# Kernel tuning notes

Measured on AMD Instinct MI355X. Metric: run time of the kernel, lower is better.

## Reference

```python
import jax, jax.numpy as jnp
import numpy as np

NUM_USERS = 200_000
NUM_ITEMS = 100_000
N = NUM_USERS + NUM_ITEMS
D = 32
E = 9_600_000
N_LAYERS = 3


def setup_inputs() -> dict:
    key = jax.random.key(0)
    k1, k2, k3, k4, k5 = jax.random.split(key, 5)
    rows = jax.random.randint(k1, (E,), 0, N, dtype=jnp.int32)
    cols = jax.random.randint(k2, (E,), 0, N, dtype=jnp.int32)
    # normalized-adjacency-like positive values
    vals = jax.random.uniform(k3, (E,), dtype=jnp.float32) * 0.05
    # xavier-uniform-ish embedding init
    bound = float(np.sqrt(6.0 / (NUM_USERS + D)))
    user_w = jax.random.uniform(k4, (NUM_USERS, D), dtype=jnp.float32,
                                minval=-bound, maxval=bound)
    bound_i = float(np.sqrt(6.0 / (NUM_ITEMS + D)))
    item_w = jax.random.uniform(k5, (NUM_ITEMS, D), dtype=jnp.float32,
                                minval=-bound_i, maxval=bound_i)
    return {"rows": rows, "cols": cols, "vals": vals,
            "user_w": user_w, "item_w": item_w}


def _spmm(rows, cols, vals, x):
    # A_hat @ x for COO A_hat: gather source features, scale, scatter-add to rows.
    msgs = vals[:, None] * x[cols]                 # [E, D]
    return jax.ops.segment_sum(msgs, rows, num_segments=N)  # [N, D]


def reference(rows, cols, vals, user_w, item_w):
    x0 = jnp.concatenate([user_w, item_w], axis=0)  # [N, D]
    x = x0
    acc = x0
    for _ in range(N_LAYERS):
        x = _spmm(rows, cols, vals, x)
        acc = acc + x
    x_mean = acc / (N_LAYERS + 1)                   # mean over layer stack
    users = x_mean[:NUM_USERS]
    items = x_mean[NUM_USERS:]
    return (users, items)
```

## Files before the change

### kernel.cpp

```cpp
#include <hip/hip_runtime.h>
#include <hip/hip_fp16.h>
#include <stdint.h>

#define NUM_USERS 200000
#define NUM_ITEMS 100000
#define NN (NUM_USERS + NUM_ITEMS)
#define D 32
#define NE 9600000
#define TOTAL (NN * D)

#define RPB2 128
#define B2 ((NN + RPB2 - 1) / RPB2)
#define CAP 5120

#define CSH 12
#define NC ((NN + (1 << CSH) - 1) >> CSH)
#define FPC 32
#define BPC 9

#define TPB_A 1024
#define EPT 16
#define EPB_A (TPB_A * EPT)

#define TPB_H 1024
#define EPT_H 32
#define EPB_H (TPB_H * EPT_H)
#define NB_H ((NE + EPB_H - 1) / EPB_H)

__global__ __launch_bounds__(256) void init_x_acc(
    const float4* __restrict__ user_w, const float4* __restrict__ item_w,
    ushort4* __restrict__ xh, float4* __restrict__ acc) {
    int i = blockIdx.x * 256 + threadIdx.x;
    const int total4 = TOTAL / 4;
    const int ub4 = (NUM_USERS * D) / 4;
    if (i < total4) {
        float4 v = (i < ub4) ? user_w[i] : item_w[i - ub4];
        acc[i] = v;
        ushort4 h;
        h.x = __half_as_ushort(__float2half(v.x));
        h.y = __half_as_ushort(__float2half(v.y));
        h.z = __half_as_ushort(__float2half(v.z));
        h.w = __half_as_ushort(__float2half(v.w));
        xh[i] = h;
    }
}

__global__ __launch_bounds__(TPB_H) void bucket_hist(
    const int4* __restrict__ rows4, int* __restrict__ bcounts) {
    __shared__ int hist[B2];
    int tid = threadIdx.x;
    for (int i = tid; i < B2; i += TPB_H) hist[i] = 0;
    __syncthreads();
    int base4 = blockIdx.x * (EPB_H / 4);
    #pragma unroll
    for (int k = 0; k < EPT_H / 4; ++k) {
        int i4 = base4 + k * TPB_H + tid;
        if (i4 < NE / 4) {
            int4 r = rows4[i4];
            atomicAdd(&hist[r.x >> 7], 1);
            atomicAdd(&hist[r.y >> 7], 1);
            atomicAdd(&hist[r.z >> 7], 1);
            atomicAdd(&hist[r.w >> 7], 1);
        }
    }
    __syncthreads();
    for (int b = tid; b < B2; b += TPB_H) {
        int c = hist[b];
        if (c) atomicAdd(&bcounts[b], c);
    }
}

__global__ __launch_bounds__(1024) void scan_buckets(
    const int* __restrict__ bcounts, int* __restrict__ bstart,
    int* __restrict__ bfill, int* __restrict__ cfill) {
    __shared__ int lds[1024];
    int t = threadIdx.x;
    int v[4];
    int s = 0;
    #pragma unroll
    for (int k = 0; k < 4; ++k) {
        int b = t * 4 + k;
        v[k] = (b < B2) ? bcounts[b] : 0;
        s += v[k];
    }
    lds[t] = s;
    __syncthreads();
    for (int off = 1; off < 1024; off <<= 1) {
        int u = (t >= off) ? lds[t - off] : 0;
        __syncthreads();
        lds[t] += u;
        __syncthreads();
    }
    int ex = lds[t] - s;
    #pragma unroll
    for (int k = 0; k < 4; ++k) {
        int b = t * 4 + k;
        if (b < B2) {
            bstart[b] = ex;
            bfill[b] = ex;
            if ((b & (FPC - 1)) == 0) cfill[b >> 5] = ex;
        }
        ex += v[k];
    }
    if (t == 1023) bstart[B2] = ex;
}

__global__ __launch_bounds__(TPB_A) void partition_coarse(
    const int4* __restrict__ rows4, const int4* __restrict__ cols4,
    const float4* __restrict__ vals4, int* __restrict__ cfill,
    int2* __restrict__ temp1) {
    __shared__ int2 stage[EPB_A];
    __shared__ int hist[NC];
    __shared__ int bnd[NC + 1];
    __shared__ int dlt[NC];
    __shared__ int sc[128];
    int tid = threadIdx.x;
    if (tid < NC) hist[tid] = 0;
    __syncthreads();

    int base4 = blockIdx.x * (EPB_A / 4);
    int keys[EPT]; int vls[EPT]; int crk[EPT];

    #pragma unroll
    for (int k = 0; k < EPT / 4; ++k) {
        int i4 = base4 + k * TPB_A + tid;
        if (i4 < NE / 4) {
            int4 r = rows4[i4];
            int4 c = cols4[i4];
            float4 v = vals4[i4];
            int c0 = r.x >> CSH, c1 = r.y >> CSH, c2 = r.z >> CSH, c3 = r.w >> CSH;
            keys[k*4+0] = ((r.x & 4095) << 19) | c.x; vls[k*4+0] = __float_as_int(v.x);
            crk[k*4+0] = (c0 << 13) | atomicAdd(&hist[c0], 1);
            keys[k*4+1] = ((r.y & 4095) << 19) | c.y; vls[k*4+1] = __float_as_int(v.y);
            crk[k*4+1] = (c1 << 13) | atomicAdd(&hist[c1], 1);
            keys[k*4+2] = ((r.z & 4095) << 19) | c.z; vls[k*4+2] = __float_as_int(v.z);
            crk[k*4+2] = (c2 << 13) | atomicAdd(&hist[c2], 1);
            keys[k*4+3] = ((r.w & 4095) << 19) | c.w; vls[k*4+3] = __float_as_int(v.w);
            crk[k*4+3] = (c3 << 13) | atomicAdd(&hist[c3], 1);
        }
    }
    __syncthreads();
    if (tid < 128) sc[tid] = (tid < NC) ? hist[tid] : 0;
    __syncthreads();
    #pragma unroll
    for (int off = 1; off < 128; off <<= 1) {
        int u = (tid >= off && tid < 128) ? sc[tid - off] : 0;
        __syncthreads();
        if (tid < 128) sc[tid] += u;
        __syncthreads();
    }
    if (tid < NC) {
        int cnt = hist[tid];
        int ex = sc[tid] - cnt;
        bnd[tid] = ex;
        dlt[tid] = (cnt ? atomicAdd(&cfill[tid], cnt) : 0) - ex;
    }
    if (tid == 0) bnd[NC] = sc[NC - 1];
    __syncthreads();
    #pragma unroll
    for (int k = 0; k < EPT / 4; ++k) {
        int i4 = base4 + k * TPB_A + tid;
        if (i4 < NE / 4) {
            #pragma unroll
            for (int j = 0; j < 4; ++j) {
                int e = k * 4 + j;
                int p = bnd[crk[e] >> 13] + (crk[e] & 0x1FFF);
                stage[p] = make_int2(keys[e], vls[e]);
            }
        }
    }
    __syncthreads();
    int ntot = bnd[NC];
    for (int j = tid; j < ntot; j += TPB_A) {
        int lo = 0, hi = NC;
        while (hi - lo > 1) { int mid = (lo + hi) >> 1; if (bnd[mid] <= j) lo = mid; else hi = mid; }
        temp1[j + dlt[lo]] = stage[j];
    }
}

__global__ __launch_bounds__(TPB_A) void partition_fine(
    const int2* __restrict__ temp1, const int* __restrict__ bstart,
    int* __restrict__ bfill, int2* __restrict__ colval) {
    __shared__ int2 stage[EPB_A];
    __shared__ int hist[FPC];
    __shared__ int bnd[FPC + 1];
    __shared__ int dlt[FPC];
    __shared__ int sc[FPC];
    int c = blockIdx.x / BPC;
    int seg = blockIdx.x % BPC;
    int cs = bstart[c * FPC];
    int ce = bstart[min((c + 1) * FPC, B2)];
    int base = cs + seg * EPB_A;
    int n = ce - base;
    if (n <= 0) return;
    if (n > EPB_A) n = EPB_A;
    int tid = threadIdx.x;
    if (tid < FPC) hist[tid] = 0;
    __syncthreads();
    int keys[EPT]; int vls[EPT]; int frk[EPT];
    #pragma unroll
    for (int k = 0; k < EPT; ++k) {
        int idx = k * TPB_A + tid;
        if (idx < n) {
            int2 e = temp1[base + idx];
            int f = (e.x >> 26) & 31;
            keys[k] = e.x; vls[k] = e.y;
            frk[k] = (f << 13) | atomicAdd(&hist[f], 1);
        }
    }
    __syncthreads();
    if (tid < FPC) sc[tid] = hist[tid];
    __syncthreads();
    #pragma unroll
    for (int off = 1; off < FPC; off <<= 1) {
        int u = (tid >= off && tid < FPC) ? sc[tid - off] : 0;
        __syncthreads();
        if (tid < FPC) sc[tid] += u;
        __syncthreads();
    }
    if (tid < FPC) {
        int cnt = hist[tid];
        int ex = sc[tid] - cnt;
        bnd[tid] = ex;
        dlt[tid] = (cnt ? atomicAdd(&bfill[c * FPC + tid], cnt) : 0) - ex;
    }
    if (tid == 0) bnd[FPC] = sc[FPC - 1];
    __syncthreads();
    #pragma unroll
    for (int k = 0; k < EPT; ++k) {
        int idx = k * TPB_A + tid;
        if (idx < n) {
            int p = bnd[frk[k] >> 13] + (frk[k] & 0x1FFF);
            int rl = (keys[k] >> 19) & 127;
            stage[p] = make_int2((rl << 19) | (keys[k] & 0x7FFFF), vls[k]);
        }
    }
    __syncthreads();
    for (int j = tid; j < n; j += TPB_A) {
        int lo = 0, hi = FPC;
        while (hi - lo > 1) { int mid = (lo + hi) >> 1; if (bnd[mid] <= j) lo = mid; else hi = mid; }
        colval[j + dlt[lo]] = stage[j];
    }
}

__global__ __launch_bounds__(256) void sort_bucket2(
    const int* __restrict__ bstart, int* __restrict__ row_start,
    int2* __restrict__ colval, int2* __restrict__ scratch) {
    __shared__ int2 stage[CAP];
    __shared__ int lstart[RPB2];
    __shared__ int lfill[RPB2];
    int b = blockIdx.x;
    int row0 = b * RPB2;
    int rcount = NN - row0; if (rcount > RPB2) rcount = RPB2;
    int tid = threadIdx.x;
    int s = bstart[b];
    int count = bstart[b + 1] - s;

    if (tid < RPB2) lfill[tid] = 0;
    __syncthreads();

    for (int i = tid; i < count; i += 256) {
        int rl = colval[s + i].x >> 19;
        atomicAdd(&lfill[rl], 1);
    }
    __syncthreads();

    int val = (tid < RPB2) ? lfill[tid] : 0;
    if (tid < RPB2) lstart[tid] = val;
    __syncthreads();
    for (int off = 1; off < RPB2; off <<= 1) {
        int u = (tid >= off && tid < RPB2) ? lstart[tid - off] : 0;
        __syncthreads();
        if (tid < RPB2) lstart[tid] += u;
        __syncthreads();
    }
    int ex = (tid < RPB2) ? lstart[tid] - val : 0;
    if (tid < RPB2) {
        lstart[tid] = ex;
        lfill[tid] = 0;
        if (tid < rcount) row_start[row0 + tid] = s + ex;
    }
    if (b == 0 && tid == 0) row_start[NN] = NE;
    __syncthreads();

    if (count <= CAP) {
        for (int i = tid; i < count; i += 256) {
            int2 e = colval[s + i];
            int rl = e.x >> 19;
            int pos = lstart[rl] + atomicAdd(&lfill[rl], 1);
            stage[pos] = make_int2(e.x & 0x7FFFF, e.y);
        }
        __syncthreads();
        for (int i = tid; i < count; i += 256) colval[s + i] = stage[i];
    } else {
        for (int i = tid; i < count; i += 256) scratch[s + i] = colval[s + i];
        __syncthreads();
        for (int i = tid; i < count; i += 256) {
            int2 e = scratch[s + i];
            int rl = e.x >> 19;
            int pos = lstart[rl] + atomicAdd(&lfill[rl], 1);
            colval[s + pos] = make_int2(e.x & 0x7FFFF, e.y);
        }
    }
}

template <bool LAST>
__global__ __launch_bounds__(256) void spmm_csr(
    const int* __restrict__ row_start, const int2* __restrict__ colval,
    const __half* __restrict__ xh, __half* __restrict__ yh,
    float* __restrict__ acc) {
    int lane = threadIdx.x & 63;
    int grp = lane >> 3;
    int fq = lane & 7;
    int row = (blockIdx.x * 256 + threadIdx.x) >> 6;
    if (row >= NN) return;
    int s = row_start[row];
    int e = row_start[row + 1];
    if (s == e) {
        if (lane < 8) {
            size_t idx = (size_t)row * D + lane * 4;
            if (!LAST) *(uint2*)(yh + idx) = make_uint2(0u, 0u);
            float4 av = *(const float4*)(acc + idx);
            if (LAST) { av.x *= 0.25f; av.y *= 0.25f; av.z *= 0.25f; av.w *= 0.25f; }
            *(float4*)(acc + idx) = av;
        }
        return;
    }
    float a0 = 0.f, a1 = 0.f, a2 = 0.f, a3 = 0.f;
    float b0 = 0.f, b1 = 0.f, b2 = 0.f, b3 = 0.f;
    int i = s;
    for (; i + 16 <= e; i += 16) {
        int2 cvA = colval[i + grp];
        int2 cvB = colval[i + 8 + grp];
        uint2 hA = *(const uint2*)(xh + (size_t)cvA.x * D + fq * 4);
        uint2 hB = *(const uint2*)(xh + (size_t)cvB.x * D + fq * 4);
        float vA = __int_as_float(cvA.y);
        float vB = __int_as_float(cvB.y);
        float2 fA0 = __half22float2(*(__half2*)&hA.x);
        float2 fA1 = __half22float2(*(__half2*)&hA.y);
        float2 fB0 = __half22float2(*(__half2*)&hB.x);
        float2 fB1 = __half22float2(*(__half2*)&hB.y);
        a0 += vA * fA0.x; a1 += vA * fA0.y; a2 += vA * fA1.x; a3 += vA * fA1.y;
        b0 += vB * fB0.x; b1 += vB * fB0.y; b2 += vB * fB1.x; b3 += vB * fB1.y;
    }
    if (i < e) {
        int iA = i + grp;
        int iB = i + 8 + grp;
        int cA = (iA < e) ? iA : (e - 1);
        int cB = (iB < e) ? iB : (e - 1);
        int2 cvA = colval[cA];
        int2 cvB = colval[cB];
        uint2 hA = *(const uint2*)(xh + (size_t)cvA.x * D + fq * 4);
        uint2 hB = *(const uint2*)(xh + (size_t)cvB.x * D + fq * 4);
        float vA = (iA < e) ? __int_as_float(cvA.y) : 0.f;
        float vB = (iB < e) ? __int_as_float(cvB.y) : 0.f;
        float2 fA0 = __half22float2(*(__half2*)&hA.x);
        float2 fA1 = __half22float2(*(__half2*)&hA.y);
        float2 fB0 = __half22float2(*(__half2*)&hB.x);
        float2 fB1 = __half22float2(*(__half2*)&hB.y);
        a0 += vA * fA0.x; a1 += vA * fA0.y; a2 += vA * fA1.x; a3 += vA * fA1.y;
        b0 += vB * fB0.x; b1 += vB * fB0.y; b2 += vB * fB1.x; b3 += vB * fB1.y;
    }
    a0 += b0; a1 += b1; a2 += b2; a3 += b3;
    #pragma unroll
    for (int m = 8; m <= 32; m <<= 1) {
        a0 += __shfl_xor(a0, m, 64);
        a1 += __shfl_xor(a1, m, 64);
        a2 += __shfl_xor(a2, m, 64);
        a3 += __shfl_xor(a3, m, 64);
    }
    if (lane < 8) {
        size_t idx = (size_t)row * D + lane * 4;
        if (!LAST) {
            __half2 h01 = __float22half2_rn(make_float2(a0, a1));
            __half2 h23 = __float22half2_rn(make_float2(a2, a3));
            *(uint2*)(yh + idx) =
                make_uint2(*(uint32_t*)&h01, *(uint32_t*)&h23);
        }
        float4 av = *(const float4*)(acc + idx);
        av.x += a0; av.y += a1; av.z += a2; av.w += a3;
        if (LAST) { av.x *= 0.25f; av.y *= 0.25f; av.z *= 0.25f; av.w *= 0.25f; }
        *(float4*)(acc + idx) = av;
    }
}

extern "C" void kernel_launch(void* const* d_in, const int* in_sizes, int n_in,
                              void* d_out, int out_size, void* d_ws, size_t ws_size,
                              hipStream_t stream) {
    const int*   rows   = (const int*)d_in[0];
    const int*   cols   = (const int*)d_in[1];
    const float* vals   = (const float*)d_in[2];
    const float* user_w = (const float*)d_in[3];
    const float* item_w = (const float*)d_in[4];

    float* acc = (float*)d_out;

    __half* xh = (__half*)d_ws;
    __half* yh = xh + (size_t)TOTAL;
    int2*  temp1 = (int2*)d_ws;
    int2*  colval = (int2*)((char*)d_ws + 2ull * (size_t)TOTAL * sizeof(float));
    int*   bcounts = (int*)(colval + (size_t)NE);
    int*   bstart = bcounts + B2;
    int*   bfill = bstart + (B2 + 1);
    int*   cfill = bfill + B2;
    int*   row_start = cfill + NC;

    const int vec_blocks   = (TOTAL / 4 + 255) / 256;
    const int partA_blocks = (NE + EPB_A - 1) / EPB_A;
    const int partF_blocks = NC * BPC;
    const int row_blocks   = (NN + 3) / 4;

    hipMemsetAsync(bcounts, 0, (size_t)B2 * sizeof(int), stream);
    bucket_hist<<<NB_H, TPB_H, 0, stream>>>((const int4*)rows, bcounts);
    scan_buckets<<<1, 1024, 0, stream>>>(bcounts, bstart, bfill, cfill);
    partition_coarse<<<partA_blocks, TPB_A, 0, stream>>>(
        (const int4*)rows, (const int4*)cols, (const float4*)vals, cfill, temp1);
    partition_fine<<<partF_blocks, TPB_A, 0, stream>>>(
        (const int2*)temp1, bstart, bfill, colval);
    sort_bucket2<<<B2, 256, 0, stream>>>(bstart, row_start, colval, temp1);

    init_x_acc<<<vec_blocks, 256, 0, stream>>>(
        (const float4*)user_w, (const float4*)item_w, (ushort4*)xh, (float4*)acc);

    spmm_csr<false><<<row_blocks, 256, 0, stream>>>(row_start, colval, xh, yh, acc);
    spmm_csr<false><<<row_blocks, 256, 0, stream>>>(row_start, colval, yh, xh, acc);
    spmm_csr<true ><<<row_blocks, 256, 0, stream>>>(row_start, colval, xh, yh, acc);
}
```

Baseline: 826.2 us.

## Store per-layer fp16 outputs and compute layer mean in a final kernel

SpMM layers no longer read-modify-write an fp32 accumulator. Each layer writes its own fp16 output buffer, and a new finalize kernel sums the four layers and scales by 1/4. The gather loop is widened to process 32 edges per iteration with nontemporal loads for column/value pairs. This cuts per-layer accumulator traffic and raises memory-level parallelism. In exchange, the initial embeddings are now rounded to fp16 before the mean, and an extra kernel launch is added.

```diff
diff --git a/kernel.cpp b/kernel.cpp
--- a/kernel.cpp
+++ b/kernel.cpp
@@ -27,21 +27,20 @@
 #define EPB_H (TPB_H * EPT_H)
 #define NB_H ((NE + EPB_H - 1) / EPB_H)
 
-__global__ __launch_bounds__(256) void init_x_acc(
+__global__ __launch_bounds__(256) void init_x0(
     const float4* __restrict__ user_w, const float4* __restrict__ item_w,
-    ushort4* __restrict__ xh, float4* __restrict__ acc) {
+    ushort4* __restrict__ x0h) {
     int i = blockIdx.x * 256 + threadIdx.x;
     const int total4 = TOTAL / 4;
     const int ub4 = (NUM_USERS * D) / 4;
     if (i < total4) {
         float4 v = (i < ub4) ? user_w[i] : item_w[i - ub4];
-        acc[i] = v;
         ushort4 h;
         h.x = __half_as_ushort(__float2half(v.x));
         h.y = __half_as_ushort(__float2half(v.y));
         h.z = __half_as_ushort(__float2half(v.z));
         h.w = __half_as_ushort(__float2half(v.w));
-        xh[i] = h;
+        x0h[i] = h;
     }
 }
 
@@ -304,11 +303,13 @@
     }
 }
 
-template <bool LAST>
+__device__ __forceinline__ float2 h2f(uint32_t u) {
+    return __half22float2(*(__half2*)&u);
+}
+
 __global__ __launch_bounds__(256) void spmm_csr(
     const int* __restrict__ row_start, const int2* __restrict__ colval,
-    const __half* __restrict__ xh, __half* __restrict__ yh,
-    float* __restrict__ acc) {
+    const __half* __restrict__ xh, __half* __restrict__ yh) {
     int lane = threadIdx.x & 63;
     int grp = lane >> 3;
     int fq = lane & 7;
@@ -316,52 +317,60 @@
     if (row >= NN) return;
     int s = row_start[row];
     int e = row_start[row + 1];
-    if (s == e) {
-        if (lane < 8) {
-            size_t idx = (size_t)row * D + lane * 4;
-            if (!LAST) *(uint2*)(yh + idx) = make_uint2(0u, 0u);
-            float4 av = *(const float4*)(acc + idx);
-            if (LAST) { av.x *= 0.25f; av.y *= 0.25f; av.z *= 0.25f; av.w *= 0.25f; }
-            *(float4*)(acc + idx) = av;
-        }
-        return;
-    }
+    const int64_t* cv8 = (const int64_t*)colval;
     float a0 = 0.f, a1 = 0.f, a2 = 0.f, a3 = 0.f;
-    float b0 = 0.f, b1 = 0.f, b2 = 0.f, b3 = 0.f;
     int i = s;
-    for (; i + 16 <= e; i += 16) {
-        int2 cvA = colval[i + grp];
-        int2 cvB = colval[i + 8 + grp];
-        uint2 hA = *(const uint2*)(xh + (size_t)cvA.x * D + fq * 4);
-        uint2 hB = *(const uint2*)(xh + (size_t)cvB.x * D + fq * 4);
-        float vA = __int_as_float(cvA.y);
-        float vB = __int_as_float(cvB.y);
-        float2 fA0 = __half22float2(*(__half2*)&hA.x);
-        float2 fA1 = __half22float2(*(__half2*)&hA.y);
-        float2 fB0 = __half22float2(*(__half2*)&hB.x);
-        float2 fB1 = __half22float2(*(__half2*)&hB.y);
-        a0 += vA * fA0.x; a1 += vA * fA0.y; a2 += vA * fA1.x; a3 += vA * fA1.y;
-        b0 += vB * fB0.x; b1 += vB * fB0.y; b2 += vB * fB1.x; b3 += vB * fB1.y;
+    for (; i + 32 <= e; i += 32) {
+        int64_t p0 = __builtin_nontemporal_load(&cv8[i + grp]);
+        int64_t p1 = __builtin_nontemporal_load(&cv8[i + 8 + grp]);
+        int64_t p2 = __builtin_nontemporal_load(&cv8[i + 16 + grp]);
+        int64_t p3 = __builtin_nontemporal_load(&cv8[i + 24 + grp]);
+        uint2 h0 = *(const uint2*)(xh + (size_t)(uint32_t)p0 * D + fq * 4);
+        uint2 h1 = *(const uint2*)(xh + (size_t)(uint32_t)p1 * D + fq * 4);
+        uint2 h2 = *(const uint2*)(xh + (size_t)(uint32_t)p2 * D + fq * 4);
+        uint2 h3 = *(const uint2*)(xh + (size_t)(uint32_t)p3 * D + fq * 4);
+        float v0 = __int_as_float((int)(p0 >> 32));
+        float v1 = __int_as_float((int)(p1 >> 32));
+        float v2 = __int_as_float((int)(p2 >> 32));
+        float v3 = __int_as_float((int)(p3 >> 32));
+        float2 f;
+        f = h2f(h0.x); a0 += v0 * f.x; a1 += v0 * f.y;
+        f = h2f(h0.y); a2 += v0 * f.x; a3 += v0 * f.y;
+        f = h2f(h1.x); a0 += v1 * f.x; a1 += v1 * f.y;
+        f = h2f(h1.y); a2 += v1 * f.x; a3 += v1 * f.y;
+        f = h2f(h2.x); a0 += v2 * f.x; a1 += v2 * f.y;
+        f = h2f(h2.y); a2 += v2 * f.x; a3 += v2 * f.y;
+        f = h2f(h3.x); a0 += v3 * f.x; a1 += v3 * f.y;
+        f = h2f(h3.y); a2 += v3 * f.x; a3 += v3 * f.y;
     }
     if (i < e) {
-        int iA = i + grp;
-        int iB = i + 8 + grp;
-        int cA = (iA < e) ? iA : (e - 1);
-        int cB = (iB < e) ? iB : (e - 1);
-        int2 cvA = colval[cA];
-        int2 cvB = colval[cB];
-        uint2 hA = *(const uint2*)(xh + (size_t)cvA.x * D + fq * 4);
-        uint2 hB = *(const uint2*)(xh + (size_t)cvB.x * D + fq * 4);
-        float vA = (iA < e) ? __int_as_float(cvA.y) : 0.f;
-        float vB = (iB < e) ? __int_as_float(cvB.y) : 0.f;
-        float2 fA0 = __half22float2(*(__half2*)&hA.x);
-        float2 fA1 = __half22float2(*(__half2*)&hA.y);
-        float2 fB0 = __half22float2(*(__half2*)&hB.x);
-        float2 fB1 = __half22float2(*(__half2*)&hB.y);
-        a0 += vA * fA0.x; a1 += vA * fA0.y; a2 += vA * fA1.x; a3 += vA * fA1.y;
-        b0 += vB * fB0.x; b1 += vB * fB0.y; b2 += vB * fB1.x; b3 += vB * fB1.y;
-    }
-    a0 += b0; a1 += b1; a2 += b2; a3 += b3;
+        int last = e - 1;
+        int i0 = i + grp,      c0 = (i0 < e) ? i0 : last;
+        int i1 = i + 8 + grp,  c1 = (i1 < e) ? i1 : last;
+        int i2 = i + 16 + grp, c2 = (i2 < e) ? i2 : last;
+        int i3 = i + 24 + grp, c3 = (i3 < e) ? i3 : last;
+        int64_t p0 = __builtin_nontemporal_load(&cv8[c0]);
+        int64_t p1 = __builtin_nontemporal_load(&cv8[c1]);
+        int64_t p2 = __builtin_nontemporal_load(&cv8[c2]);
+        int64_t p3 = __builtin_nontemporal_load(&cv8[c3]);
+        uint2 h0 = *(const uint2*)(xh + (size_t)(uint32_t)p0 * D + fq * 4);
+        uint2 h1 = *(const uint2*)(xh + (size_t)(uint32_t)p1 * D + fq * 4);
+        uint2 h2 = *(const uint2*)(xh + (size_t)(uint32_t)p2 * D + fq * 4);
+        uint2 h3 = *(const uint2*)(xh + (size_t)(uint32_t)p3 * D + fq * 4);
+        float v0 = (i0 < e) ? __int_as_float((int)(p0 >> 32)) : 0.f;
+        float v1 = (i1 < e) ? __int_as_float((int)(p1 >> 32)) : 0.f;
+        float v2 = (i2 < e) ? __int_as_float((int)(p2 >> 32)) : 0.f;
+        float v3 = (i3 < e) ? __int_as_float((int)(p3 >> 32)) : 0.f;
+        float2 f;
+        f = h2f(h0.x); a0 += v0 * f.x; a1 += v0 * f.y;
+        f = h2f(h0.y); a2 += v0 * f.x; a3 += v0 * f.y;
+        f = h2f(h1.x); a0 += v1 * f.x; a1 += v1 * f.y;
+        f = h2f(h1.y); a2 += v1 * f.x; a3 += v1 * f.y;
+        f = h2f(h2.x); a0 += v2 * f.x; a1 += v2 * f.y;
+        f = h2f(h2.y); a2 += v2 * f.x; a3 += v2 * f.y;
+        f = h2f(h3.x); a0 += v3 * f.x; a1 += v3 * f.y;
+        f = h2f(h3.y); a2 += v3 * f.x; a3 += v3 * f.y;
+    }
     #pragma unroll
     for (int m = 8; m <= 32; m <<= 1) {
         a0 += __shfl_xor(a0, m, 64);
@@ -371,17 +380,30 @@
     }
     if (lane < 8) {
         size_t idx = (size_t)row * D + lane * 4;
-        if (!LAST) {
-            __half2 h01 = __float22half2_rn(make_float2(a0, a1));
-            __half2 h23 = __float22half2_rn(make_float2(a2, a3));
-            *(uint2*)(yh + idx) =
-                make_uint2(*(uint32_t*)&h01, *(uint32_t*)&h23);
-        }
-        float4 av = *(const float4*)(acc + idx);
-        av.x += a0; av.y += a1; av.z += a2; av.w += a3;
-        if (LAST) { av.x *= 0.25f; av.y *= 0.25f; av.z *= 0.25f; av.w *= 0.25f; }
-        *(float4*)(acc + idx) = av;
-    }
+        __half2 h01 = __float22half2_rn(make_float2(a0, a1));
+        __half2 h23 = __float22half2_rn(make_float2(a2, a3));
+        *(uint2*)(yh + idx) = make_uint2(*(uint32_t*)&h01, *(uint32_t*)&h23);
+    }
+}
+
+__global__ __launch_bounds__(256) void finalize_mean(
+    const uint4* __restrict__ x0, const uint4* __restrict__ x1,
+    const uint4* __restrict__ x2, const uint4* __restrict__ x3,
+    float4* __restrict__ acc) {
+    int i = blockIdx.x * 256 + threadIdx.x;
+    if (i >= TOTAL / 8) return;
+    uint4 a = x0[i], b = x1[i], c = x2[i], d = x3[i];
+    float2 s0, s1, s2, s3, t;
+    s0 = h2f(a.x); t = h2f(b.x); s0.x += t.x; s0.y += t.y;
+    t = h2f(c.x); s0.x += t.x; s0.y += t.y; t = h2f(d.x); s0.x += t.x; s0.y += t.y;
+    s1 = h2f(a.y); t = h2f(b.y); s1.x += t.x; s1.y += t.y;
+    t = h2f(c.y); s1.x += t.x; s1.y += t.y; t = h2f(d.y); s1.x += t.x; s1.y += t.y;
+    s2 = h2f(a.z); t = h2f(b.z); s2.x += t.x; s2.y += t.y;
+    t = h2f(c.z); s2.x += t.x; s2.y += t.y; t = h2f(d.z); s2.x += t.x; s2.y += t.y;
+    s3 = h2f(a.w); t = h2f(b.w); s3.x += t.x; s3.y += t.y;
+    t = h2f(c.w); s3.x += t.x; s3.y += t.y; t = h2f(d.w); s3.x += t.x; s3.y += t.y;
+    acc[2 * i]     = make_float4(s0.x * 0.25f, s0.y * 0.25f, s1.x * 0.25f, s1.y * 0.25f);
+    acc[2 * i + 1] = make_float4(s2.x * 0.25f, s2.y * 0.25f, s3.x * 0.25f, s3.y * 0.25f);
 }
 
 extern "C" void kernel_launch(void* const* d_in, const int* in_sizes, int n_in,
@@ -395,8 +417,10 @@
 
     float* acc = (float*)d_out;
 
-    __half* xh = (__half*)d_ws;
-    __half* yh = xh + (size_t)TOTAL;
+    __half* x0h = (__half*)d_ws;
+    __half* x1h = x0h + (size_t)TOTAL;
+    __half* x2h = x1h + (size_t)TOTAL;
+    __half* x3h = x2h + (size_t)TOTAL;
     int2*  temp1 = (int2*)d_ws;
     int2*  colval = (int2*)((char*)d_ws + 2ull * (size_t)TOTAL * sizeof(float));
     int*   bcounts = (int*)(colval + (size_t)NE);
@@ -406,6 +430,7 @@
     int*   row_start = cfill + NC;
 
     const int vec_blocks   = (TOTAL / 4 + 255) / 256;
+    const int mean_blocks  = (TOTAL / 8 + 255) / 256;
     const int partA_blocks = (NE + EPB_A - 1) / EPB_A;
     const int partF_blocks = NC * BPC;
     const int row_blocks   = (NN + 3) / 4;
@@ -419,10 +444,14 @@
         (const int2*)temp1, bstart, bfill, colval);
     sort_bucket2<<<B2, 256, 0, stream>>>(bstart, row_start, colval, temp1);
 
-    init_x_acc<<<vec_blocks, 256, 0, stream>>>(
-        (const float4*)user_w, (const float4*)item_w, (ushort4*)xh, (float4*)acc);
-
-    spmm_csr<false><<<row_blocks, 256, 0, stream>>>(row_start, colval, xh, yh, acc);
-    spmm_csr<false><<<row_blocks, 256, 0, stream>>>(row_start, colval, yh, xh, acc);
-    spmm_csr<true ><<<row_blocks, 256, 0, stream>>>(row_start, colval, xh, yh, acc);
-}
+    init_x0<<<vec_blocks, 256, 0, stream>>>(
+        (const float4*)user_w, (const float4*)item_w, (ushort4*)x0h);
+
+    spmm_csr<<<row_blocks, 256, 0, stream>>>(row_start, colval, x0h, x1h);
+    spmm_csr<<<row_blocks, 256, 0, stream>>>(row_start, colval, x1h, x2h);
+    spmm_csr<<<row_blocks, 256, 0, stream>>>(row_start, colval, x2h, x3h);
+
+    finalize_mean<<<mean_blocks, 256, 0, stream>>>(
+        (const uint4*)x0h, (const uint4*)x1h, (const uint4*)x2h,
+        (const uint4*)x3h, (float4*)acc);
+}
```

After: 808.4 us. -2.2%, faster.
